# Kernel optimization log

Measured on AMD Instinct MI355X. Metric: run time of the kernel, lower is better.

The kernel has to match this reference:

```python
import jax, jax.numpy as jnp
import numpy as np

IN_FEATURES = 4096
OUT_FEATURES = 11008
TOKENS = 8192


def setup_inputs() -> dict:
    key = jax.random.key(0)
    k_x, k_w, k_s, k_b = jax.random.split(key, 4)
    x = jax.random.normal(k_x, (TOKENS, IN_FEATURES), dtype=jnp.float32)
    # symmetric int8 weights in [-127, 127]
    qweight = jax.random.randint(k_w, (OUT_FEATURES, IN_FEATURES), -127, 128, dtype=jnp.int32).astype(jnp.int8)
    # per-output-channel positive scale (abs-max / 127 style)
    weight_scale = jax.random.uniform(k_s, (OUT_FEATURES, 1), dtype=jnp.float32, minval=1e-4, maxval=0.02)
    bias = jax.random.normal(k_b, (OUT_FEATURES,), dtype=jnp.float32)
    return {"x": x, "qweight": qweight, "weight_scale": weight_scale, "bias": bias}


def reference(x, qweight, weight_scale, bias):
    # dequantize: [out, in] fp weight = int8 * per-row scale, cast to x dtype
    weight = (qweight.astype(jnp.float32) * weight_scale).astype(x.dtype)
    # F.linear: x @ weight.T + bias
    out = jnp.einsum("ti,oi->to", x, weight) + bias.astype(x.dtype)
    return out
```

## Files before the change

### kernel.cpp

```cpp
#include <hip/hip_runtime.h>
#include <stdint.h>


#define TOKENS 8192
#define IN_F   4096
#define OUT_F  11008

#define BM 256
#define BN 256
#define BK 128
#define KT   (IN_F / BK)
#define MBLK (TOKENS / BM)
#define NBLK (OUT_F / BN)
#define NWG  (MBLK * NBLK)

static_assert(NWG % 8 == 0, "XCD swizzle requires nwg % 8 == 0");
static_assert(KT % 2 == 0, "double-buffer parity");

#define LDS_BUF   65536
#define LDS_TOTAL 131072

typedef __attribute__((ext_vector_type(4))) float f32x4;
typedef __attribute__((ext_vector_type(4))) int   i32x4;

__device__ __forceinline__ void gload_lds16(const void* g, void* l) {
  typedef const __attribute__((address_space(1))) unsigned int* gp_t;
  typedef __attribute__((address_space(3))) unsigned int* lp_t;
  __builtin_amdgcn_global_load_lds((gp_t)g, (lp_t)l, 16, 0, 0);
}

#define MFMA(d, a, b) \
  asm("v_mfma_i32_16x16x64_i8 %0, %1, %2, %0" : "+v"(d) : "v"(a), "v"(b))

#define BARRIER __builtin_amdgcn_s_barrier()
#define LGKM0                                                  \
  do {                                                         \
    asm volatile("s_waitcnt lgkmcnt(0)" ::: "memory");         \
    __builtin_amdgcn_sched_barrier(0);                         \
  } while (0)
#define VMW_(N) asm volatile("s_waitcnt vmcnt(" #N ")" ::: "memory")
#define VMW(N) VMW_(N)

__global__ __launch_bounds__(256) void quant_x_kernel(
    const float* __restrict__ x, signed char* __restrict__ xq,
    float* __restrict__ sx) {
  const int row = blockIdx.x;
  const int tid = threadIdx.x;
  const float* xr = x + (size_t)row * IN_F;
  f32x4 v[4];
#pragma unroll
  for (int p = 0; p < 4; ++p) v[p] = ((const f32x4*)xr)[tid + 256 * p];
  float am = 0.f;
#pragma unroll
  for (int p = 0; p < 4; ++p)
#pragma unroll
    for (int j = 0; j < 4; ++j) am = fmaxf(am, fabsf(v[p][j]));
#pragma unroll
  for (int off = 32; off; off >>= 1) am = fmaxf(am, __shfl_xor(am, off, 64));
  __shared__ float wmax[4];
  if ((tid & 63) == 0) wmax[tid >> 6] = am;
  __syncthreads();
  am = fmaxf(fmaxf(wmax[0], wmax[1]), fmaxf(wmax[2], wmax[3]));
  const float inv = (am > 0.f) ? 127.0f / am : 0.f;
  if (tid == 0) sx[row] = (am > 0.f) ? am / 127.0f : 1.0f;
  int* xqi = (int*)(xq + (size_t)row * IN_F);
#pragma unroll
  for (int p = 0; p < 4; ++p) {
    int pk = 0;
#pragma unroll
    for (int j = 0; j < 4; ++j) {
      int q = (int)rintf(v[p][j] * inv);
      pk |= (q & 0xff) << (8 * j);
    }
    xqi[tid + 256 * p] = pk;
  }
}

__global__ void cvt_w_kernel(const int* __restrict__ w,
                             signed char* __restrict__ wq, int n16) {
  int i = blockIdx.x * blockDim.x + threadIdx.x;
  int stride = gridDim.x * blockDim.x;
  for (int c = i; c < n16; c += stride) {
    const i32x4* src = (const i32x4*)w + (size_t)c * 4;
    i32x4 outv;
#pragma unroll
    for (int q = 0; q < 4; ++q) {
      i32x4 v = src[q];
      outv[q] = (v[0] & 0xff) | ((v[1] & 0xff) << 8) |
                ((v[2] & 0xff) << 16) | (v[3] << 24);
    }
    ((i32x4*)wq)[c] = outv;
  }
}

__global__ __launch_bounds__(512) void gemm_i8_kernel(
    const signed char* __restrict__ A,
    const signed char* __restrict__ Bm,
    const float* __restrict__ sx,
    const float* __restrict__ scale,
    const float* __restrict__ bias,
    float* __restrict__ C)
{
  extern __shared__ char lds[];

  const int tid  = threadIdx.x;
  const int lane = tid & 63;
  const int wave = tid >> 6;
  const int wm   = wave >> 2;
  const int wn   = wave & 3;
  const int grp  = lane >> 4;
  const int rsel = lane & 15;

  int bid = blockIdx.x;
  int wg  = (bid & 7) * (NWG / 8) + (bid >> 3);
  const int m_idx = wg % MBLK;
  const int n_idx = wg / MBLK;
  const int row0 = m_idx * BM;
  const int col0 = n_idx * BN;

  const int r0  = tid >> 3;
  const int jg  = (tid & 7) ^ (r0 & 7);
  const int gAL0 = r0;
  const int gAL1 = 128 + r0;
  const int gBL0 = r0 + (r0 & 32);
  const int gBL1 = 128 + r0 + (r0 & 32);
  const signed char* pAL0 = A  + (size_t)(row0 + gAL0) * IN_F + jg * 16;
  const signed char* pAL1 = A  + (size_t)(row0 + gAL1) * IN_F + jg * 16;
  const signed char* pAH0 = pAL0 + (size_t)64 * IN_F;
  const signed char* pAH1 = pAL1 + (size_t)64 * IN_F;
  const signed char* pBL0 = Bm + (size_t)(col0 + gBL0) * IN_F + jg * 16;
  const signed char* pBL1 = Bm + (size_t)(col0 + gBL1) * IN_F + jg * 16;
  const signed char* pBH0 = pBL0 + (size_t)32 * IN_F;
  const signed char* pBH1 = pBL1 + (size_t)32 * IN_F;
  const int stBase = wave * 1024;

  auto stALBL = [&](int bo, int t2) {
    const int ko = t2 * BK;
    gload_lds16(pAL0 + ko, lds + bo + 0     + stBase);
    gload_lds16(pAL1 + ko, lds + bo + 8192  + stBase);
    gload_lds16(pBL0 + ko, lds + bo + 32768 + stBase);
    gload_lds16(pBL1 + ko, lds + bo + 40960 + stBase);
  };
  auto stBH = [&](int bo, int t2) {
    const int ko = t2 * BK;
    gload_lds16(pBH0 + ko, lds + bo + 49152 + stBase);
    gload_lds16(pBH1 + ko, lds + bo + 57344 + stBase);
  };
  auto stAH = [&](int bo, int t2) {
    const int ko = t2 * BK;
    gload_lds16(pAH0 + ko, lds + bo + 16384 + stBase);
    gload_lds16(pAH1 + ko, lds + bo + 24576 + stBase);
  };

  const int swz0  = (grp ^ (rsel & 7)) << 4;
  const int swz1  = swz0 ^ 64;
  const int aBase = wm * 8192 + rsel * 128;
  const int bBase = wn * 4096 + rsel * 128;

  i32x4 zero = {0, 0, 0, 0};
  i32x4 acc[8][4];
#pragma unroll
  for (int m = 0; m < 8; ++m)
#pragma unroll
    for (int n = 0; n < 4; ++n) acc[m][n] = zero;

#define DS_AL(BO, MI, SW) (*(const i32x4*)(lds + (BO) + 0     + aBase + (MI)*2048 + (SW)))
#define DS_AH(BO, MI, SW) (*(const i32x4*)(lds + (BO) + 16384 + aBase + (MI)*2048 + (SW)))
#define DS_BL(BO, NI, SW) (*(const i32x4*)(lds + (BO) + 32768 + bBase + (NI)*2048 + (SW)))
#define DS_BH(BO, NI, SW) (*(const i32x4*)(lds + (BO) + 49152 + bBase + (NI)*2048 + (SW)))

#define TILE(BO, T, DO_STAGE, W0, W1, W3)                                      \
  {                                                                            \
    i32x4 arLo[8], arHi[8], brLo[4], brHi[4];                                  \
                                 \
    _Pragma("unroll") for (int m = 0; m < 4; ++m) {                            \
      arLo[m * 2]     = DS_AL(BO, m, swz0);                                    \
      arLo[m * 2 + 1] = DS_AL(BO, m, swz1);                                    \
    }                                                                          \
    _Pragma("unroll") for (int n = 0; n < 2; ++n) {                            \
      brLo[n * 2]     = DS_BL(BO, n, swz0);                                    \
      brLo[n * 2 + 1] = DS_BL(BO, n, swz1);                                    \
    }                                                                          \
    LGKM0;                                                                     \
    __builtin_amdgcn_s_setprio(1);                                             \
    _Pragma("unroll") for (int m = 0; m < 4; ++m)                              \
      _Pragma("unroll") for (int n = 0; n < 2; ++n)                            \
        _Pragma("unroll") for (int kk = 0; kk < 2; ++kk)                       \
          MFMA(acc[m][n], arLo[m * 2 + kk], brLo[n * 2 + kk]);                 \
    __builtin_amdgcn_s_setprio(0);                                             \
    VMW(W0);                                                                   \
    BARRIER;                                                                   \
                       \
    _Pragma("unroll") for (int n = 0; n < 2; ++n) {                            \
      brHi[n * 2]     = DS_BH(BO, n, swz0);                                    \
      brHi[n * 2 + 1] = DS_BH(BO, n, swz1);                                    \
    }                                                                          \
    if (DO_STAGE) stALBL((BO), (T) + 2);                                       \
    LGKM0;                                                                     \
    __builtin_amdgcn_s_setprio(1);                                             \
    _Pragma("unroll") for (int m = 0; m < 4; ++m)                              \
      _Pragma("unroll") for (int n = 0; n < 2; ++n)                            \
        _Pragma("unroll") for (int kk = 0; kk < 2; ++kk)                       \
          MFMA(acc[m][n + 2], arLo[m * 2 + kk], brHi[n * 2 + kk]);             \
    __builtin_amdgcn_s_setprio(0);                                             \
    VMW(W1);                                                                   \
    BARRIER;                                                                   \
                          \
    _Pragma("unroll") for (int m = 0; m < 4; ++m) {                            \
      arHi[m * 2]     = DS_AH(BO, m, swz0);                                    \
      arHi[m * 2 + 1] = DS_AH(BO, m, swz1);                                    \
    }                                                                          \
    if (DO_STAGE) stBH((BO), (T) + 2);                                         \
    LGKM0;                                                                     \
    __builtin_amdgcn_s_setprio(1);                                             \
    _Pragma("unroll") for (int m = 0; m < 4; ++m)                              \
      _Pragma("unroll") for (int n = 0; n < 2; ++n)                            \
        _Pragma("unroll") for (int kk = 0; kk < 2; ++kk)                       \
          MFMA(acc[m + 4][n + 2], arHi[m * 2 + kk], brHi[n * 2 + kk]);         \
    __builtin_amdgcn_s_setprio(0);                                             \
    BARRIER;                                                                   \
                      \
    if (DO_STAGE) stAH((BO), (T) + 2);                                         \
    __builtin_amdgcn_s_setprio(1);                                             \
    _Pragma("unroll") for (int m = 0; m < 4; ++m)                              \
      _Pragma("unroll") for (int n = 0; n < 2; ++n)                            \
        _Pragma("unroll") for (int kk = 0; kk < 2; ++kk)                       \
          MFMA(acc[m + 4][n], arHi[m * 2 + kk], brLo[n * 2 + kk]);             \
    __builtin_amdgcn_s_setprio(0);                                             \
    VMW(W3);                                                                   \
    BARRIER;                                                                   \
  }

  stALBL(0, 0);
  stBH(0, 0);
  stAH(0, 0);
  stALBL(LDS_BUF, 1);
  stBH(LDS_BUF, 1);
  stAH(LDS_BUF, 1);
  VMW(12);
  BARRIER;

  for (int t2 = 0; t2 < KT - 2; t2 += 2) {
    TILE(0,       t2,     true, 10, 12, 12);
    TILE(LDS_BUF, t2 + 1, true, 10, 12, 12);
  }
  TILE(0,       KT - 2, false, 10, 8, 4);
  TILE(LDS_BUF, KT - 1, false, 2, 0, 0);

#undef TILE
#undef DS_AL
#undef DS_AH
#undef DS_BL
#undef DS_BH

  asm volatile("s_nop 7\n\ts_nop 7" :::);

#pragma unroll
  for (int n = 0; n < 4; ++n) {
    int o = col0 + wn * 64 + n * 16 + rsel;
    float s  = scale[o];
    float bz = bias[o];
#pragma unroll
    for (int m = 0; m < 8; ++m) {
      int tr = row0 + wm * 128 + m * 16 + grp * 4;
      const f32x4 sxv = *(const f32x4*)(sx + tr);
      float* cp = C + (size_t)tr * OUT_F + o;
      i32x4 v = acc[m][n];
      cp[0 * (size_t)OUT_F] = (float)v[0] * (sxv[0] * s) + bz;
      cp[1 * (size_t)OUT_F] = (float)v[1] * (sxv[1] * s) + bz;
      cp[2 * (size_t)OUT_F] = (float)v[2] * (sxv[2] * s) + bz;
      cp[3 * (size_t)OUT_F] = (float)v[3] * (sxv[3] * s) + bz;
    }
  }
}

__global__ void gemm_naive_kernel(const float* __restrict__ x,
                                  const int* __restrict__ w,
                                  const float* __restrict__ sc,
                                  const float* __restrict__ bs,
                                  float* __restrict__ out) {
  long long idx = (long long)blockIdx.x * blockDim.x + threadIdx.x;
  long long total = (long long)TOKENS * OUT_F;
  if (idx >= total) return;
  int t = (int)(idx / OUT_F);
  int o = (int)(idx % OUT_F);
  const float* xp = x + (size_t)t * IN_F;
  const int* wp = w + (size_t)o * IN_F;
  float acc = 0.f;
  for (int k = 0; k < IN_F; k += 4) {
    i32x4 wv = *(const i32x4*)(wp + k);
    f32x4 xv = *(const f32x4*)(xp + k);
    acc += xv[0] * (float)wv[0] + xv[1] * (float)wv[1]
         + xv[2] * (float)wv[2] + xv[3] * (float)wv[3];
  }
  out[idx] = acc * sc[o] + bs[o];
}

extern "C" void kernel_launch(void* const* d_in, const int* in_sizes, int n_in,
                              void* d_out, int out_size, void* d_ws, size_t ws_size,
                              hipStream_t stream) {
  const float* x  = (const float*)d_in[0];
  const int*   qw = (const int*)d_in[1];
  const float* sc = (const float*)d_in[2];
  const float* bs = (const float*)d_in[3];
  float* out = (float*)d_out;

  const size_t xqBytes = (size_t)TOKENS * IN_F;
  const size_t wqBytes = (size_t)OUT_F * IN_F;
  const size_t sxBytes = (size_t)TOKENS * sizeof(float);

  if (ws_size >= xqBytes + wqBytes + sxBytes) {
    signed char* xq = (signed char*)d_ws;
    signed char* wq = (signed char*)((char*)d_ws + xqBytes);
    float*       sx = (float*)((char*)d_ws + xqBytes + wqBytes);
    quant_x_kernel<<<TOKENS, 256, 0, stream>>>(x, xq, sx);
    cvt_w_kernel<<<2048, 256, 0, stream>>>(qw, wq, OUT_F * IN_F / 16);
    (void)hipFuncSetAttribute((const void*)gemm_i8_kernel,
                              hipFuncAttributeMaxDynamicSharedMemorySize,
                              LDS_TOTAL);
    gemm_i8_kernel<<<NWG, 512, LDS_TOTAL, stream>>>(xq, wq, sx, sc, bs, out);
  } else {
    long long total = (long long)TOKENS * OUT_F;
    int blocks = (int)((total + 255) / 256);
    gemm_naive_kernel<<<blocks, 256, 0, stream>>>(x, qw, sc, bs, out);
  }
}
```

Baseline: 516.2 us.

## Halve K tile to 64 with new LDS swizzle and loader mapping

Cuts the K-step of the int8 MFMA GEMM from 128 to 64, which halves the double-buffered LDS footprint from 128KB to 64KB. The global-to-LDS load mapping, the LDS swizzle and the ds_read addressing are reworked for 64-byte rows, and the vmcnt wait counts are rescaled to match. The smaller LDS use could allow two workgroups per CU and so better latency hiding. In exchange there are twice as many barrier-separated iterations and less MFMA work between syncs.

```diff
diff --git a/kernel.cpp b/kernel.cpp
--- a/kernel.cpp
+++ b/kernel.cpp
@@ -8,7 +8,7 @@
 
 #define BM 256
 #define BN 256
-#define BK 128
+#define BK 64
 #define KT   (IN_F / BK)
 #define MBLK (TOKENS / BM)
 #define NBLK (OUT_F / BN)
@@ -17,8 +17,8 @@
 static_assert(NWG % 8 == 0, "XCD swizzle requires nwg % 8 == 0");
 static_assert(KT % 2 == 0, "double-buffer parity");
 
-#define LDS_BUF   65536
-#define LDS_TOTAL 131072
+#define LDS_BUF   32768
+#define LDS_TOTAL 65536
 
 typedef __attribute__((ext_vector_type(4))) float f32x4;
 typedef __attribute__((ext_vector_type(4))) int   i32x4;
@@ -40,6 +40,8 @@
   } while (0)
 #define VMW_(N) asm volatile("s_waitcnt vmcnt(" #N ")" ::: "memory")
 #define VMW(N) VMW_(N)
+#define PRIO1 __builtin_amdgcn_s_setprio(1)
+#define PRIO0 __builtin_amdgcn_s_setprio(0)
 
 __global__ __launch_bounds__(256) void quant_x_kernel(
     const float* __restrict__ x, signed char* __restrict__ xq,
@@ -118,44 +120,34 @@
   const int row0 = m_idx * BM;
   const int col0 = n_idx * BN;
 
-  const int r0  = tid >> 3;
-  const int jg  = (tid & 7) ^ (r0 & 7);
-  const int gAL0 = r0;
-  const int gAL1 = 128 + r0;
-  const int gBL0 = r0 + (r0 & 32);
-  const int gBL1 = 128 + r0 + (r0 & 32);
-  const signed char* pAL0 = A  + (size_t)(row0 + gAL0) * IN_F + jg * 16;
-  const signed char* pAL1 = A  + (size_t)(row0 + gAL1) * IN_F + jg * 16;
-  const signed char* pAH0 = pAL0 + (size_t)64 * IN_F;
-  const signed char* pAH1 = pAL1 + (size_t)64 * IN_F;
-  const signed char* pBL0 = Bm + (size_t)(col0 + gBL0) * IN_F + jg * 16;
-  const signed char* pBL1 = Bm + (size_t)(col0 + gBL1) * IN_F + jg * 16;
-  const signed char* pBH0 = pBL0 + (size_t)32 * IN_F;
-  const signed char* pBH1 = pBL1 + (size_t)32 * IN_F;
+  const int Lmod  = (tid >> 3) & 7;
+  const int slog  = (tid & 7) ^ Lmod;
+  const int rreg  = 2 * (tid >> 3) + (slog >> 2);
+  const int colOf = (slog & 3) * 16;
+  const int gA = (rreg & 63) | ((rreg & 64) << 1);
+  const int gB = (rreg & 31) | ((rreg & 96) << 1);
+  const signed char* pA0 = A  + (size_t)(row0 + gA) * IN_F + colOf;
+  const signed char* pA1 = pA0 + (size_t)64 * IN_F;
+  const signed char* pB0 = Bm + (size_t)(col0 + gB) * IN_F + colOf;
+  const signed char* pB1 = pB0 + (size_t)32 * IN_F;
   const int stBase = wave * 1024;
 
   auto stALBL = [&](int bo, int t2) {
     const int ko = t2 * BK;
-    gload_lds16(pAL0 + ko, lds + bo + 0     + stBase);
-    gload_lds16(pAL1 + ko, lds + bo + 8192  + stBase);
-    gload_lds16(pBL0 + ko, lds + bo + 32768 + stBase);
-    gload_lds16(pBL1 + ko, lds + bo + 40960 + stBase);
+    gload_lds16(pA0 + ko, lds + bo + 0     + stBase);
+    gload_lds16(pB0 + ko, lds + bo + 16384 + stBase);
   };
   auto stBH = [&](int bo, int t2) {
-    const int ko = t2 * BK;
-    gload_lds16(pBH0 + ko, lds + bo + 49152 + stBase);
-    gload_lds16(pBH1 + ko, lds + bo + 57344 + stBase);
+    gload_lds16(pB1 + t2 * BK, lds + bo + 24576 + stBase);
   };
   auto stAH = [&](int bo, int t2) {
-    const int ko = t2 * BK;
-    gload_lds16(pAH0 + ko, lds + bo + 16384 + stBase);
-    gload_lds16(pAH1 + ko, lds + bo + 24576 + stBase);
+    gload_lds16(pA1 + t2 * BK, lds + bo + 8192 + stBase);
   };
 
-  const int swz0  = (grp ^ (rsel & 7)) << 4;
-  const int swz1  = swz0 ^ 64;
-  const int aBase = wm * 8192 + rsel * 128;
-  const int bBase = wn * 4096 + rsel * 128;
+  const int sphysR = ((rsel & 1) * 4 + grp) ^ (rsel >> 1);
+  const int fOffC  = (rsel >> 1) * 128 + sphysR * 16;
+  const int aBase  = wm * 4096 + fOffC;
+  const int bBase  = 16384 + wn * 2048 + fOffC;
 
   i32x4 zero = {0, 0, 0, 0};
   i32x4 acc[8][4];
@@ -164,69 +156,53 @@
 #pragma unroll
     for (int n = 0; n < 4; ++n) acc[m][n] = zero;
 
-#define DS_AL(BO, MI, SW) (*(const i32x4*)(lds + (BO) + 0     + aBase + (MI)*2048 + (SW)))
-#define DS_AH(BO, MI, SW) (*(const i32x4*)(lds + (BO) + 16384 + aBase + (MI)*2048 + (SW)))
-#define DS_BL(BO, NI, SW) (*(const i32x4*)(lds + (BO) + 32768 + bBase + (NI)*2048 + (SW)))
-#define DS_BH(BO, NI, SW) (*(const i32x4*)(lds + (BO) + 49152 + bBase + (NI)*2048 + (SW)))
-
-#define TILE(BO, T, DO_STAGE, W0, W1, W3)                                      \
+#define DS_A(BO, MI) \
+  (*(const i32x4*)(lds + (BO) + ((MI) & 3) * 1024 + ((MI) >> 2) * 8192 + aBase))
+#define DS_B(BO, NI) \
+  (*(const i32x4*)(lds + (BO) + ((NI) & 1) * 1024 + ((NI) >> 1) * 8192 + bBase))
+
+#define TILE(BO, T, STG, W0, W1, W3)                                           \
   {                                                                            \
-    i32x4 arLo[8], arHi[8], brLo[4], brHi[4];                                  \
+    i32x4 arLo[4], arHi[4], brLo[2], brHi[2];                                  \
                                  \
-    _Pragma("unroll") for (int m = 0; m < 4; ++m) {                            \
-      arLo[m * 2]     = DS_AL(BO, m, swz0);                                    \
-      arLo[m * 2 + 1] = DS_AL(BO, m, swz1);                                    \
-    }                                                                          \
-    _Pragma("unroll") for (int n = 0; n < 2; ++n) {                            \
-      brLo[n * 2]     = DS_BL(BO, n, swz0);                                    \
-      brLo[n * 2 + 1] = DS_BL(BO, n, swz1);                                    \
-    }                                                                          \
+    _Pragma("unroll") for (int m = 0; m < 4; ++m) arLo[m] = DS_A(BO, m);       \
+    _Pragma("unroll") for (int n = 0; n < 2; ++n) brLo[n] = DS_B(BO, n);       \
     LGKM0;                                                                     \
-    __builtin_amdgcn_s_setprio(1);                                             \
+    PRIO1;                                                                     \
     _Pragma("unroll") for (int m = 0; m < 4; ++m)                              \
       _Pragma("unroll") for (int n = 0; n < 2; ++n)                            \
-        _Pragma("unroll") for (int kk = 0; kk < 2; ++kk)                       \
-          MFMA(acc[m][n], arLo[m * 2 + kk], brLo[n * 2 + kk]);                 \
-    __builtin_amdgcn_s_setprio(0);                                             \
+        MFMA(acc[m][n], arLo[m], brLo[n]);                                     \
+    PRIO0;                                                                     \
     VMW(W0);                                                                   \
     BARRIER;                                                                   \
-                       \
-    _Pragma("unroll") for (int n = 0; n < 2; ++n) {                            \
-      brHi[n * 2]     = DS_BH(BO, n, swz0);                                    \
-      brHi[n * 2 + 1] = DS_BH(BO, n, swz1);                                    \
-    }                                                                          \
-    if (DO_STAGE) stALBL((BO), (T) + 2);                                       \
+                        \
+    _Pragma("unroll") for (int n = 0; n < 2; ++n) brHi[n] = DS_B(BO, n + 2);   \
+    if (STG) stALBL((BO), (T) + 2);                                            \
     LGKM0;                                                                     \
-    __builtin_amdgcn_s_setprio(1);                                             \
+    PRIO1;                                                                     \
     _Pragma("unroll") for (int m = 0; m < 4; ++m)                              \
       _Pragma("unroll") for (int n = 0; n < 2; ++n)                            \
-        _Pragma("unroll") for (int kk = 0; kk < 2; ++kk)                       \
-          MFMA(acc[m][n + 2], arLo[m * 2 + kk], brHi[n * 2 + kk]);             \
-    __builtin_amdgcn_s_setprio(0);                                             \
+        MFMA(acc[m][n + 2], arLo[m], brHi[n]);                                 \
+    PRIO0;                                                                     \
     VMW(W1);                                                                   \
     BARRIER;                                                                   \
                           \
-    _Pragma("unroll") for (int m = 0; m < 4; ++m) {                            \
-      arHi[m * 2]     = DS_AH(BO, m, swz0);                                    \
-      arHi[m * 2 + 1] = DS_AH(BO, m, swz1);                                    \
-    }                                                                          \
-    if (DO_STAGE) stBH((BO), (T) + 2);                                         \
+    _Pragma("unroll") for (int m = 0; m < 4; ++m) arHi[m] = DS_A(BO, m + 4);   \
+    if (STG) stBH((BO), (T) + 2);                                              \
     LGKM0;                                                                     \
-    __builtin_amdgcn_s_setprio(1);                                             \
+    PRIO1;                                                                     \
     _Pragma("unroll") for (int m = 0; m < 4; ++m)                              \
       _Pragma("unroll") for (int n = 0; n < 2; ++n)                            \
-        _Pragma("unroll") for (int kk = 0; kk < 2; ++kk)                       \
-          MFMA(acc[m + 4][n + 2], arHi[m * 2 + kk], brHi[n * 2 + kk]);         \
-    __builtin_amdgcn_s_setprio(0);                                             \
+        MFMA(acc[m + 4][n + 2], arHi[m], brHi[n]);                             \
+    PRIO0;                                                                     \
     BARRIER;                                                                   \
                       \
-    if (DO_STAGE) stAH((BO), (T) + 2);                                         \
-    __builtin_amdgcn_s_setprio(1);                                             \
+    if (STG) stAH((BO), (T) + 2);                                              \
+    PRIO1;                                                                     \
     _Pragma("unroll") for (int m = 0; m < 4; ++m)                              \
       _Pragma("unroll") for (int n = 0; n < 2; ++n)                            \
-        _Pragma("unroll") for (int kk = 0; kk < 2; ++kk)                       \
-          MFMA(acc[m + 4][n], arHi[m * 2 + kk], brLo[n * 2 + kk]);             \
-    __builtin_amdgcn_s_setprio(0);                                             \
+        MFMA(acc[m + 4][n], arHi[m], brLo[n]);                                 \
+    PRIO0;                                                                     \
     VMW(W3);                                                                   \
     BARRIER;                                                                   \
   }
@@ -237,21 +213,19 @@
   stALBL(LDS_BUF, 1);
   stBH(LDS_BUF, 1);
   stAH(LDS_BUF, 1);
-  VMW(12);
+  VMW(6);
   BARRIER;
 
   for (int t2 = 0; t2 < KT - 2; t2 += 2) {
-    TILE(0,       t2,     true, 10, 12, 12);
-    TILE(LDS_BUF, t2 + 1, true, 10, 12, 12);
-  }
-  TILE(0,       KT - 2, false, 10, 8, 4);
-  TILE(LDS_BUF, KT - 1, false, 2, 0, 0);
+    TILE(0,       t2,     true, 5, 6, 6);
+    TILE(LDS_BUF, t2 + 1, true, 5, 6, 6);
+  }
+  TILE(0,       KT - 2, false, 5, 4, 2);
+  TILE(LDS_BUF, KT - 1, false, 1, 0, 0);
 
 #undef TILE
-#undef DS_AL
-#undef DS_AH
-#undef DS_BL
-#undef DS_BH
+#undef DS_A
+#undef DS_B
 
   asm volatile("s_nop 7\n\ts_nop 7" :::);
 
```

New measurement: 570.3 us. 10.5% more time.

## Restructure int8 GEMM tile pipeline into two phases with fewer barriers

Applied to the files above, without the earlier changes.

Reorganizes the per-K-tile schedule of the int8 MFMA GEMM from four barrier-separated quadrants into two halves. All B fragments and the low A half are read up front, and the next tile's A-high stage is issued into the other buffer earlier, which shifts the prefetch schedule and vmcnt wait counts. The goal is to halve barrier synchronisation and give longer MFMA runs between waits. In exchange it holds more live registers and has a more intricate staging and wait order that must stay race-free.

```diff
diff --git a/kernel.cpp b/kernel.cpp
--- a/kernel.cpp
+++ b/kernel.cpp
@@ -40,6 +40,8 @@
   } while (0)
 #define VMW_(N) asm volatile("s_waitcnt vmcnt(" #N ")" ::: "memory")
 #define VMW(N) VMW_(N)
+#define PRIO1 __builtin_amdgcn_s_setprio(1)
+#define PRIO0 __builtin_amdgcn_s_setprio(0)
 
 __global__ __launch_bounds__(256) void quant_x_kernel(
     const float* __restrict__ x, signed char* __restrict__ xq,
@@ -169,10 +171,10 @@
 #define DS_BL(BO, NI, SW) (*(const i32x4*)(lds + (BO) + 32768 + bBase + (NI)*2048 + (SW)))
 #define DS_BH(BO, NI, SW) (*(const i32x4*)(lds + (BO) + 49152 + bBase + (NI)*2048 + (SW)))
 
-#define TILE(BO, T, DO_STAGE, W0, W1, W3)                                      \
+#define TILE(BO, T, STG_A, STG_B, G0, G1)                                      \
   {                                                                            \
     i32x4 arLo[8], arHi[8], brLo[4], brHi[4];                                  \
-                                 \
+                \
     _Pragma("unroll") for (int m = 0; m < 4; ++m) {                            \
       arLo[m * 2]     = DS_AL(BO, m, swz0);                                    \
       arLo[m * 2 + 1] = DS_AL(BO, m, swz1);                                    \
@@ -180,54 +182,41 @@
     _Pragma("unroll") for (int n = 0; n < 2; ++n) {                            \
       brLo[n * 2]     = DS_BL(BO, n, swz0);                                    \
       brLo[n * 2 + 1] = DS_BL(BO, n, swz1);                                    \
+      brHi[n * 2]     = DS_BH(BO, n, swz0);                                    \
+      brHi[n * 2 + 1] = DS_BH(BO, n, swz1);                                    \
     }                                                                          \
+    if (STG_A) stAH((BO) ^ LDS_BUF, (T) + 1);                                  \
     LGKM0;                                                                     \
-    __builtin_amdgcn_s_setprio(1);                                             \
+    PRIO1;                                                                     \
     _Pragma("unroll") for (int m = 0; m < 4; ++m)                              \
       _Pragma("unroll") for (int n = 0; n < 2; ++n)                            \
         _Pragma("unroll") for (int kk = 0; kk < 2; ++kk)                       \
           MFMA(acc[m][n], arLo[m * 2 + kk], brLo[n * 2 + kk]);                 \
-    __builtin_amdgcn_s_setprio(0);                                             \
-    VMW(W0);                                                                   \
-    BARRIER;                                                                   \
-                       \
-    _Pragma("unroll") for (int n = 0; n < 2; ++n) {                            \
-      brHi[n * 2]     = DS_BH(BO, n, swz0);                                    \
-      brHi[n * 2 + 1] = DS_BH(BO, n, swz1);                                    \
-    }                                                                          \
-    if (DO_STAGE) stALBL((BO), (T) + 2);                                       \
-    LGKM0;                                                                     \
-    __builtin_amdgcn_s_setprio(1);                                             \
     _Pragma("unroll") for (int m = 0; m < 4; ++m)                              \
       _Pragma("unroll") for (int n = 0; n < 2; ++n)                            \
         _Pragma("unroll") for (int kk = 0; kk < 2; ++kk)                       \
           MFMA(acc[m][n + 2], arLo[m * 2 + kk], brHi[n * 2 + kk]);             \
-    __builtin_amdgcn_s_setprio(0);                                             \
-    VMW(W1);                                                                   \
+    PRIO0;                                                                     \
+    VMW(G0);                                                                   \
     BARRIER;                                                                   \
-                          \
+                       \
     _Pragma("unroll") for (int m = 0; m < 4; ++m) {                            \
       arHi[m * 2]     = DS_AH(BO, m, swz0);                                    \
       arHi[m * 2 + 1] = DS_AH(BO, m, swz1);                                    \
     }                                                                          \
-    if (DO_STAGE) stBH((BO), (T) + 2);                                         \
+    if (STG_B) { stALBL((BO), (T) + 2); stBH((BO), (T) + 2); }                 \
     LGKM0;                                                                     \
-    __builtin_amdgcn_s_setprio(1);                                             \
+    PRIO1;                                                                     \
     _Pragma("unroll") for (int m = 0; m < 4; ++m)                              \
       _Pragma("unroll") for (int n = 0; n < 2; ++n)                            \
         _Pragma("unroll") for (int kk = 0; kk < 2; ++kk)                       \
           MFMA(acc[m + 4][n + 2], arHi[m * 2 + kk], brHi[n * 2 + kk]);         \
-    __builtin_amdgcn_s_setprio(0);                                             \
-    BARRIER;                                                                   \
-                      \
-    if (DO_STAGE) stAH((BO), (T) + 2);                                         \
-    __builtin_amdgcn_s_setprio(1);                                             \
     _Pragma("unroll") for (int m = 0; m < 4; ++m)                              \
       _Pragma("unroll") for (int n = 0; n < 2; ++n)                            \
         _Pragma("unroll") for (int kk = 0; kk < 2; ++kk)                       \
           MFMA(acc[m + 4][n], arHi[m * 2 + kk], brLo[n * 2 + kk]);             \
-    __builtin_amdgcn_s_setprio(0);                                             \
-    VMW(W3);                                                                   \
+    PRIO0;                                                                     \
+    VMW(G1);                                                                   \
     BARRIER;                                                                   \
   }
 
@@ -236,16 +225,15 @@
   stAH(0, 0);
   stALBL(LDS_BUF, 1);
   stBH(LDS_BUF, 1);
-  stAH(LDS_BUF, 1);
-  VMW(12);
+  VMW(8);
   BARRIER;
 
-  for (int t2 = 0; t2 < KT - 2; t2 += 2) {
-    TILE(0,       t2,     true, 10, 12, 12);
-    TILE(LDS_BUF, t2 + 1, true, 10, 12, 12);
-  }
-  TILE(0,       KT - 2, false, 10, 8, 4);
-  TILE(LDS_BUF, KT - 1, false, 2, 0, 0);
+  for (int t2 = 0; t2 <= KT - 4; t2 += 2) {
+    TILE(0,       t2,     1, 1, 8, 8);
+    TILE(LDS_BUF, t2 + 1, 1, 1, 8, 8);
+  }
+  TILE(0,       KT - 2, 1, 0, 8, 2);
+  TILE(LDS_BUF, KT - 1, 0, 0, 0, 0);
 
 #undef TILE
 #undef DS_AL
```

New measurement: 523.4 us. About the same (+1.4%).

## Switch int8 GEMM inner loop to 32x32x32 MFMA instruction

Applied to the files above, without the earlier changes.

Replaces the 16x16x64 int8 MFMA with the 32x32x32 variant. Each wave now holds 4x2 tiles of 32x32 with 16-element accumulators. LDS read offsets and the swizzle are reworked to match the new operand layout, and the epilogue is remapped to the 32x32 output layout. Larger MFMA tiles are meant to cut LDS operand reads per FLOP and instruction issue overhead, at the cost of new bank-conflict behavior and a changed swizzle that must stay correct.

```diff
diff --git a/kernel.cpp b/kernel.cpp
--- a/kernel.cpp
+++ b/kernel.cpp
@@ -20,8 +20,9 @@
 #define LDS_BUF   65536
 #define LDS_TOTAL 131072
 
-typedef __attribute__((ext_vector_type(4))) float f32x4;
-typedef __attribute__((ext_vector_type(4))) int   i32x4;
+typedef __attribute__((ext_vector_type(4)))  float f32x4;
+typedef __attribute__((ext_vector_type(4)))  int   i32x4;
+typedef __attribute__((ext_vector_type(16))) int   i32x16;
 
 __device__ __forceinline__ void gload_lds16(const void* g, void* l) {
   typedef const __attribute__((address_space(1))) unsigned int* gp_t;
@@ -29,8 +30,8 @@
   __builtin_amdgcn_global_load_lds((gp_t)g, (lp_t)l, 16, 0, 0);
 }
 
-#define MFMA(d, a, b) \
-  asm("v_mfma_i32_16x16x64_i8 %0, %1, %2, %0" : "+v"(d) : "v"(a), "v"(b))
+#define MFMA32(d, a, b) \
+  asm("v_mfma_i32_32x32x32_i8 %0, %1, %2, %0" : "+v"(d) : "v"(a), "v"(b))
 
 #define BARRIER __builtin_amdgcn_s_barrier()
 #define LGKM0                                                  \
@@ -40,6 +41,8 @@
   } while (0)
 #define VMW_(N) asm volatile("s_waitcnt vmcnt(" #N ")" ::: "memory")
 #define VMW(N) VMW_(N)
+#define PRIO1 __builtin_amdgcn_s_setprio(1)
+#define PRIO0 __builtin_amdgcn_s_setprio(0)
 
 __global__ __launch_bounds__(256) void quant_x_kernel(
     const float* __restrict__ x, signed char* __restrict__ xq,
@@ -108,8 +111,8 @@
   const int wave = tid >> 6;
   const int wm   = wave >> 2;
   const int wn   = wave & 3;
-  const int grp  = lane >> 4;
-  const int rsel = lane & 15;
+  const int l31  = lane & 31;
+  const int hi   = lane >> 5;
 
   int bid = blockIdx.x;
   int wg  = (bid & 7) * (NWG / 8) + (bid >> 3);
@@ -152,81 +155,82 @@
     gload_lds16(pAH1 + ko, lds + bo + 24576 + stBase);
   };
 
-  const int swz0  = (grp ^ (rsel & 7)) << 4;
-  const int swz1  = swz0 ^ 64;
-  const int aBase = wm * 8192 + rsel * 128;
-  const int bBase = wn * 4096 + rsel * 128;
-
-  i32x4 zero = {0, 0, 0, 0};
-  i32x4 acc[8][4];
-#pragma unroll
-  for (int m = 0; m < 8; ++m)
-#pragma unroll
-    for (int n = 0; n < 4; ++n) acc[m][n] = zero;
-
-#define DS_AL(BO, MI, SW) (*(const i32x4*)(lds + (BO) + 0     + aBase + (MI)*2048 + (SW)))
-#define DS_AH(BO, MI, SW) (*(const i32x4*)(lds + (BO) + 16384 + aBase + (MI)*2048 + (SW)))
-#define DS_BL(BO, NI, SW) (*(const i32x4*)(lds + (BO) + 32768 + bBase + (NI)*2048 + (SW)))
-#define DS_BH(BO, NI, SW) (*(const i32x4*)(lds + (BO) + 49152 + bBase + (NI)*2048 + (SW)))
+  const int lowb = (hi ^ (lane & 1)) * 16;
+  const int kx   = (lane >> 1) & 3;
+  const int swk0 = lowb + ((0 ^ kx) << 5);
+  const int swk1 = lowb + ((1 ^ kx) << 5);
+  const int swk2 = lowb + ((2 ^ kx) << 5);
+  const int swk3 = lowb + ((3 ^ kx) << 5);
+  const int aBase = (wm * 64 + l31) * 128;
+  const int bBase = (wn * 32 + l31) * 128;
+
+  i32x16 acc[4][2];
+#pragma unroll
+  for (int m = 0; m < 4; ++m)
+#pragma unroll
+    for (int n = 0; n < 2; ++n)
+#pragma unroll
+      for (int j = 0; j < 16; ++j) acc[m][n][j] = 0;
+
+#define DS_AL(BO, MI, SW) (*(const i32x4*)(lds + (BO) + 0     + aBase + (MI)*4096 + (SW)))
+#define DS_AH(BO, MI, SW) (*(const i32x4*)(lds + (BO) + 16384 + aBase + (MI)*4096 + (SW)))
+#define DS_BL(BO, SW)     (*(const i32x4*)(lds + (BO) + 32768 + bBase + (SW)))
+#define DS_BH(BO, SW)     (*(const i32x4*)(lds + (BO) + 49152 + bBase + (SW)))
 
 #define TILE(BO, T, DO_STAGE, W0, W1, W3)                                      \
   {                                                                            \
     i32x4 arLo[8], arHi[8], brLo[4], brHi[4];                                  \
-                                 \
-    _Pragma("unroll") for (int m = 0; m < 4; ++m) {                            \
-      arLo[m * 2]     = DS_AL(BO, m, swz0);                                    \
-      arLo[m * 2 + 1] = DS_AL(BO, m, swz1);                                    \
+                                                            \
+    _Pragma("unroll") for (int mf = 0; mf < 2; ++mf) {                         \
+      arLo[mf * 4 + 0] = DS_AL(BO, mf, swk0);                                  \
+      arLo[mf * 4 + 1] = DS_AL(BO, mf, swk1);                                  \
+      arLo[mf * 4 + 2] = DS_AL(BO, mf, swk2);                                  \
+      arLo[mf * 4 + 3] = DS_AL(BO, mf, swk3);                                  \
     }                                                                          \
-    _Pragma("unroll") for (int n = 0; n < 2; ++n) {                            \
-      brLo[n * 2]     = DS_BL(BO, n, swz0);                                    \
-      brLo[n * 2 + 1] = DS_BL(BO, n, swz1);                                    \
-    }                                                                          \
+    brLo[0] = DS_BL(BO, swk0); brLo[1] = DS_BL(BO, swk1);                      \
+    brLo[2] = DS_BL(BO, swk2); brLo[3] = DS_BL(BO, swk3);                      \
     LGKM0;                                                                     \
-    __builtin_amdgcn_s_setprio(1);                                             \
-    _Pragma("unroll") for (int m = 0; m < 4; ++m)                              \
-      _Pragma("unroll") for (int n = 0; n < 2; ++n)                            \
-        _Pragma("unroll") for (int kk = 0; kk < 2; ++kk)                       \
-          MFMA(acc[m][n], arLo[m * 2 + kk], brLo[n * 2 + kk]);                 \
-    __builtin_amdgcn_s_setprio(0);                                             \
+    PRIO1;                                                                     \
+    _Pragma("unroll") for (int mf = 0; mf < 2; ++mf)                           \
+      _Pragma("unroll") for (int kk = 0; kk < 4; ++kk)                         \
+        MFMA32(acc[mf][0], arLo[mf * 4 + kk], brLo[kk]);                       \
+    PRIO0;                                                                     \
     VMW(W0);                                                                   \
     BARRIER;                                                                   \
-                       \
-    _Pragma("unroll") for (int n = 0; n < 2; ++n) {                            \
-      brHi[n * 2]     = DS_BH(BO, n, swz0);                                    \
-      brHi[n * 2 + 1] = DS_BH(BO, n, swz1);                                    \
-    }                                                                          \
+                                                            \
+    brHi[0] = DS_BH(BO, swk0); brHi[1] = DS_BH(BO, swk1);                      \
+    brHi[2] = DS_BH(BO, swk2); brHi[3] = DS_BH(BO, swk3);                      \
     if (DO_STAGE) stALBL((BO), (T) + 2);                                       \
     LGKM0;                                                                     \
-    __builtin_amdgcn_s_setprio(1);                                             \
-    _Pragma("unroll") for (int m = 0; m < 4; ++m)                              \
-      _Pragma("unroll") for (int n = 0; n < 2; ++n)                            \
-        _Pragma("unroll") for (int kk = 0; kk < 2; ++kk)                       \
-          MFMA(acc[m][n + 2], arLo[m * 2 + kk], brHi[n * 2 + kk]);             \
-    __builtin_amdgcn_s_setprio(0);                                             \
+    PRIO1;                                                                     \
+    _Pragma("unroll") for (int mf = 0; mf < 2; ++mf)                           \
+      _Pragma("unroll") for (int kk = 0; kk < 4; ++kk)                         \
+        MFMA32(acc[mf][1], arLo[mf * 4 + kk], brHi[kk]);                       \
+    PRIO0;                                                                     \
     VMW(W1);                                                                   \
     BARRIER;                                                                   \
-                          \
-    _Pragma("unroll") for (int m = 0; m < 4; ++m) {                            \
-      arHi[m * 2]     = DS_AH(BO, m, swz0);                                    \
-      arHi[m * 2 + 1] = DS_AH(BO, m, swz1);                                    \
+                                                            \
+    _Pragma("unroll") for (int mf = 0; mf < 2; ++mf) {                         \
+      arHi[mf * 4 + 0] = DS_AH(BO, mf, swk0);                                  \
+      arHi[mf * 4 + 1] = DS_AH(BO, mf, swk1);                                  \
+      arHi[mf * 4 + 2] = DS_AH(BO, mf, swk2);                                  \
+      arHi[mf * 4 + 3] = DS_AH(BO, mf, swk3);                                  \
     }                                                                          \
     if (DO_STAGE) stBH((BO), (T) + 2);                                         \
     LGKM0;                                                                     \
-    __builtin_amdgcn_s_setprio(1);                                             \
-    _Pragma("unroll") for (int m = 0; m < 4; ++m)                              \
-      _Pragma("unroll") for (int n = 0; n < 2; ++n)                            \
-        _Pragma("unroll") for (int kk = 0; kk < 2; ++kk)                       \
-          MFMA(acc[m + 4][n + 2], arHi[m * 2 + kk], brHi[n * 2 + kk]);         \
-    __builtin_amdgcn_s_setprio(0);                                             \
+    PRIO1;                                                                     \
+    _Pragma("unroll") for (int mf = 0; mf < 2; ++mf)                           \
+      _Pragma("unroll") for (int kk = 0; kk < 4; ++kk)                         \
+        MFMA32(acc[mf + 2][1], arHi[mf * 4 + kk], brHi[kk]);                   \
+    PRIO0;                                                                     \
     BARRIER;                                                                   \
-                      \
+                                                            \
     if (DO_STAGE) stAH((BO), (T) + 2);                                         \
-    __builtin_amdgcn_s_setprio(1);                                             \
-    _Pragma("unroll") for (int m = 0; m < 4; ++m)                              \
-      _Pragma("unroll") for (int n = 0; n < 2; ++n)                            \
-        _Pragma("unroll") for (int kk = 0; kk < 2; ++kk)                       \
-          MFMA(acc[m + 4][n], arHi[m * 2 + kk], brLo[n * 2 + kk]);             \
-    __builtin_amdgcn_s_setprio(0);                                             \
+    PRIO1;                                                                     \
+    _Pragma("unroll") for (int mf = 0; mf < 2; ++mf)                           \
+      _Pragma("unroll") for (int kk = 0; kk < 4; ++kk)                         \
+        MFMA32(acc[mf + 2][0], arHi[mf * 4 + kk], brLo[kk]);                   \
+    PRIO0;                                                                     \
     VMW(W3);                                                                   \
     BARRIER;                                                                   \
   }
@@ -256,20 +260,24 @@
   asm volatile("s_nop 7\n\ts_nop 7" :::);
 
 #pragma unroll
-  for (int n = 0; n < 4; ++n) {
-    int o = col0 + wn * 64 + n * 16 + rsel;
+  for (int nf = 0; nf < 2; ++nf) {
+    int o = col0 + wn * 64 + nf * 32 + l31;
     float s  = scale[o];
     float bz = bias[o];
 #pragma unroll
-    for (int m = 0; m < 8; ++m) {
-      int tr = row0 + wm * 128 + m * 16 + grp * 4;
-      const f32x4 sxv = *(const f32x4*)(sx + tr);
-      float* cp = C + (size_t)tr * OUT_F + o;
-      i32x4 v = acc[m][n];
-      cp[0 * (size_t)OUT_F] = (float)v[0] * (sxv[0] * s) + bz;
-      cp[1 * (size_t)OUT_F] = (float)v[1] * (sxv[1] * s) + bz;
-      cp[2 * (size_t)OUT_F] = (float)v[2] * (sxv[2] * s) + bz;
-      cp[3 * (size_t)OUT_F] = (float)v[3] * (sxv[3] * s) + bz;
+    for (int mf = 0; mf < 4; ++mf) {
+      int rbase = row0 + wm * 128 + mf * 32 + 4 * hi;
+      i32x16 v = acc[mf][nf];
+#pragma unroll
+      for (int q = 0; q < 4; ++q) {
+        int tr = rbase + q * 8;
+        const f32x4 sxv = *(const f32x4*)(sx + tr);
+        float* cp = C + (size_t)tr * OUT_F + o;
+        cp[0 * (size_t)OUT_F] = (float)v[q * 4 + 0] * (sxv[0] * s) + bz;
+        cp[1 * (size_t)OUT_F] = (float)v[q * 4 + 1] * (sxv[1] * s) + bz;
+        cp[2 * (size_t)OUT_F] = (float)v[q * 4 + 2] * (sxv[2] * s) + bz;
+        cp[3 * (size_t)OUT_F] = (float)v[q * 4 + 3] * (sxv[3] * s) + bz;
+      }
     }
   }
 }
```

Measured after the change: 519.0 us. No clear change (+0.6%).
